# Optimization experiments

Measured on AMD Instinct MI355X. Metric: run time of the kernel, lower is better.

Reference implementation:

```python
import jax, jax.numpy as jnp
import numpy as np


def setup_inputs() -> dict:
    key = jax.random.key(0)
    k1, k2, k3, k4 = jax.random.split(key, 4)
    B, Q, D, H = 8, 512, 4096, 1024
    return {
        "query_embeddings": jax.random.normal(k1, (B, Q, H), dtype=jnp.float32),
        "document_embeddings": jax.random.normal(k2, (B, D, H), dtype=jnp.float32),
        "attention_mask": jax.random.randint(k3, (B, D), 0, 2, dtype=jnp.int32),
        "proj_w": jax.random.normal(k4, (H, H), dtype=jnp.float32) * (H ** -0.5),
        "proj_b": jnp.zeros((H,), dtype=jnp.float32),
    }


def reference(query_embeddings, document_embeddings, attention_mask, proj_w, proj_b):
    H = query_embeddings.shape[-1]
    scale = 1.0 / jnp.sqrt(jnp.asarray(H, dtype=query_embeddings.dtype))
    # Linear projection of queries: [B, Q, H]
    q = jnp.einsum("bqh,hk->bqk", query_embeddings, proj_w) + proj_b
    # Scores: [B, Q, D]
    scores = jnp.einsum("bqh,bdh->bqd", q, document_embeddings) * scale
    # Mask: [B, 1, D]; masked positions -> -inf before softmax
    mask = attention_mask[:, None, :] != 0
    scores = jnp.where(mask, scores, -jnp.inf)
    attention_weights = jax.nn.softmax(scores, axis=-1)
    # Weighted sum over docs: [B, Q, H]
    retrieved_docs = jnp.einsum("bqd,bdh->bqh", attention_weights, document_embeddings)
    return (retrieved_docs, attention_weights)
```

## Files before the change

kernel.cpp:

```cpp
#include <hip/hip_runtime.h>

#define BATCH 8
#define QLEN 512
#define DLEN 4096
#define HDIM 1024

typedef __attribute__((ext_vector_type(8))) short bf16x8;
typedef __attribute__((ext_vector_type(4))) float f32x4;
typedef __attribute__((ext_vector_type(4))) short s16x4;

__device__ __forceinline__ short f2bf(float f) {
    union { float f; unsigned u; } x; x.f = f;
    unsigned r = x.u + 0x7fffu + ((x.u >> 16) & 1u);
    return (short)(r >> 16);
}

__device__ __forceinline__ void gload_lds16(const void* g, void* l) {
    __builtin_amdgcn_global_load_lds(
        (const __attribute__((address_space(1))) unsigned int*)g,
        (__attribute__((address_space(3))) unsigned int*)l,
        16, 0, 0);
}

#define WAIT_VMCNT(n) asm volatile("s_waitcnt vmcnt(" #n ")" ::: "memory")

__global__ void cvt_f32_bf16(const float* __restrict__ in, short* __restrict__ out, int n4) {
    int i = blockIdx.x * blockDim.x + threadIdx.x;
    int stride = gridDim.x * blockDim.x;
    for (; i < n4; i += stride) {
        float4 x = ((const float4*)in)[i];
        s16x4 o = { f2bf(x.x), f2bf(x.y), f2bf(x.z), f2bf(x.w) };
        ((s16x4*)out)[i] = o;
    }
}

__global__ void transpose_w(const float* __restrict__ W, short* __restrict__ Wt) {
    __shared__ float t[32][33];
    const int hb = blockIdx.y * 32, kb = blockIdx.x * 32;
    #pragma unroll
    for (int i = 0; i < 4; ++i) {
        int h = threadIdx.y + i * 8;
        t[h][threadIdx.x] = W[(size_t)(hb + h) * HDIM + kb + threadIdx.x];
    }
    __syncthreads();
    #pragma unroll
    for (int i = 0; i < 4; ++i) {
        int k = threadIdx.y + i * 8;
        Wt[(size_t)(kb + k) * HDIM + hb + threadIdx.x] = f2bf(t[threadIdx.x][k]);
    }
}

__global__ void transpose_docs(const short* __restrict__ docsB, short* __restrict__ docsT) {
    __shared__ unsigned t[64][65];
    const int b = blockIdx.z;
    const int h0 = blockIdx.x * 64, d0 = blockIdx.y * 64;
    const int tq = threadIdx.x & 15;
    const int tr = threadIdx.x >> 4;
    #pragma unroll
    for (int i = 0; i < 4; ++i) {
        int d = tr + i * 16;
        s16x4 v = *(const s16x4*)(docsB + ((size_t)b * DLEN + d0 + d) * HDIM + h0 + tq * 4);
        t[d][tq * 4 + 0] = (unsigned short)v[0];
        t[d][tq * 4 + 1] = (unsigned short)v[1];
        t[d][tq * 4 + 2] = (unsigned short)v[2];
        t[d][tq * 4 + 3] = (unsigned short)v[3];
    }
    __syncthreads();
    #pragma unroll
    for (int i = 0; i < 4; ++i) {
        int h = tr + i * 16;
        s16x4 o = { (short)t[tq * 4 + 0][h], (short)t[tq * 4 + 1][h],
                    (short)t[tq * 4 + 2][h], (short)t[tq * 4 + 3][h] };
        *(s16x4*)(docsT + ((size_t)b * HDIM + h0 + h) * DLEN + d0 + tq * 4) = o;
    }
}

#define G1BM 128
#define G1BN 128
#define G1BK 64

__global__ void gemm128_bias(const short* __restrict__ A, const short* __restrict__ B,
                             short* __restrict__ C, const float* __restrict__ bias,
                             int N, int Kstride, int Kloop, int sx, int sxy) {
    __shared__ short As[G1BM * G1BK];
    __shared__ short Bs[G1BN * G1BK];
    const int tid  = threadIdx.x;
    const int lane = tid & 63;
    const int wv   = tid >> 6;
    const int wr   = wv >> 1, wc = wv & 1;

    const int wg = (blockIdx.x & 7) * (gridDim.x >> 3) + (blockIdx.x >> 3);
    const int bx = wg & ((1 << sx) - 1);
    const int by = (wg >> sx) & ((1 << (sxy - sx)) - 1);

    const size_t rowBase = (size_t)by * G1BM;
    const size_t colBase = (size_t)bx * G1BN;

    f32x4 acc[4][4];
    #pragma unroll
    for (int m = 0; m < 4; ++m)
        #pragma unroll
        for (int n = 0; n < 4; ++n)
            acc[m][n] = (f32x4){0.f, 0.f, 0.f, 0.f};

    const short* aSrc[4]; const short* bSrc[4]; int dOff[4];
    #pragma unroll
    for (int i = 0; i < 4; ++i) {
        const int c = tid + 256 * i;
        const int r = c >> 3, cc = c & 7;
        const int gk = (cc ^ (r & 7)) << 3;
        aSrc[i] = A + (rowBase + r) * (size_t)Kstride + gk;
        bSrc[i] = B + (colBase + r) * (size_t)Kstride + gk;
        dOff[i] = c * 8;
    }
    const int lr = lane & 15;
    const int lk = (lane >> 4) << 3;

    for (int kt = 0; kt < Kloop; kt += G1BK) {
        #pragma unroll
        for (int i = 0; i < 4; ++i) gload_lds16(aSrc[i] + kt, As + dOff[i]);
        #pragma unroll
        for (int i = 0; i < 4; ++i) gload_lds16(bSrc[i] + kt, Bs + dOff[i]);
        __syncthreads();

        #pragma unroll
        for (int kk = 0; kk < 2; ++kk) {
            const int chunkL = (kk * 32 + lk) >> 3;
            bf16x8 af[4], bfr[4];
            #pragma unroll
            for (int m = 0; m < 4; ++m) {
                const int row = wr * 64 + m * 16 + lr;
                af[m] = *(const bf16x8*)(As + row * G1BK + ((chunkL ^ (row & 7)) << 3));
            }
            #pragma unroll
            for (int n = 0; n < 4; ++n) {
                const int row = wc * 64 + n * 16 + lr;
                bfr[n] = *(const bf16x8*)(Bs + row * G1BK + ((chunkL ^ (row & 7)) << 3));
            }
            #pragma unroll
            for (int m = 0; m < 4; ++m)
                #pragma unroll
                for (int n = 0; n < 4; ++n)
                    acc[m][n] = __builtin_amdgcn_mfma_f32_16x16x32_bf16(af[m], bfr[n], acc[m][n], 0, 0, 0);
        }
        __syncthreads();
    }

    const int orow = (lane >> 4) << 2;
    const int ocol = lane & 15;
    #pragma unroll
    for (int n = 0; n < 4; ++n) {
        const size_t col = colBase + wc * 64 + n * 16 + ocol;
        const float bv = bias[col];
        #pragma unroll
        for (int m = 0; m < 4; ++m) {
            const size_t rbase = rowBase + wr * 64 + m * 16 + orow;
            #pragma unroll
            for (int j = 0; j < 4; ++j)
                C[(rbase + j) * (size_t)N + col] = f2bf(acc[m][n][j] + bv);
        }
    }
}

#define G2BM 256
#define G2BN 256
#define G2BK 32
#define G2TS (G2BM * G2BK)

template<int EPI>
__launch_bounds__(512, 1)
__global__ void gemm256(const short* __restrict__ A, const short* __restrict__ B,
                        float* __restrict__ Cv, float scale,
                        int N, int Kstride, int Kloop, int kOffStep,
                        int sx, int sxy,
                        long long aB, long long bB, long long cB) {
    __shared__ short As[3 * G2TS];
    __shared__ short Bs[3 * G2TS];
    const int tid  = threadIdx.x;
    const int lane = tid & 63;
    const int wv   = tid >> 6;
    const int wm   = wv >> 2;
    const int wn   = wv & 3;

    const int wg = (blockIdx.x & 7) * (gridDim.x >> 3) + (blockIdx.x >> 3);
    const int bx = wg & ((1 << sx) - 1);
    const int by = (wg >> sx) & ((1 << (sxy - sx)) - 1);
    const int z  = wg >> sxy;

    const size_t rowBase = (size_t)by * G2BM;
    const size_t colBase = (size_t)bx * G2BN;
    const int bb = z & 7;
    const int kOff = (z >> 3) * kOffStep;
    const short* Ag = A + (size_t)bb * aB + kOff;
    const short* Bg = B + (size_t)bb * bB + kOff;

    f32x4 acc[8][4];
    #pragma unroll
    for (int m = 0; m < 8; ++m)
        #pragma unroll
        for (int n = 0; n < 4; ++n)
            acc[m][n] = (f32x4){0.f, 0.f, 0.f, 0.f};

    const short* aSrc[2]; const short* bSrc[2]; int dOff[2];
    #pragma unroll
    for (int i = 0; i < 2; ++i) {
        const int c = tid + 512 * i;
        const int r = c >> 2, cc = c & 3;
        const int gk = (cc ^ ((r >> 1) & 3)) << 3;
        aSrc[i] = Ag + (rowBase + r) * (size_t)Kstride + gk;
        bSrc[i] = Bg + (colBase + r) * (size_t)Kstride + gk;
        dOff[i] = c * 8;
    }
    const int chunkL = lane >> 4;
    const int lr = lane & 15;

    const int nt = Kloop / G2BK;

    #pragma unroll
    for (int i = 0; i < 2; ++i) gload_lds16(aSrc[i], As + dOff[i]);
    #pragma unroll
    for (int i = 0; i < 2; ++i) gload_lds16(bSrc[i], Bs + dOff[i]);
    #pragma unroll
    for (int i = 0; i < 2; ++i) gload_lds16(aSrc[i] + G2BK, As + G2TS + dOff[i]);
    #pragma unroll
    for (int i = 0; i < 2; ++i) gload_lds16(bSrc[i] + G2BK, Bs + G2TS + dOff[i]);
    WAIT_VMCNT(4);
    __builtin_amdgcn_s_barrier();

    for (int t = 0; t < nt; ++t) {
        if (t + 2 < nt) {
            const int kt = (t + 2) * G2BK;
            const int o = ((t + 2) % 3) * G2TS;
            #pragma unroll
            for (int i = 0; i < 2; ++i) gload_lds16(aSrc[i] + kt, As + o + dOff[i]);
            #pragma unroll
            for (int i = 0; i < 2; ++i) gload_lds16(bSrc[i] + kt, Bs + o + dOff[i]);
        }

        const short* Ab = As + (t % 3) * G2TS;
        const short* Bb = Bs + (t % 3) * G2TS;
        bf16x8 bfr[4], af[8];
        #pragma unroll
        for (int n = 0; n < 4; ++n) {
            const int row = wn * 64 + n * 16 + lr;
            bfr[n] = *(const bf16x8*)(Bb + row * G2BK + ((chunkL ^ ((row >> 1) & 3)) << 3));
        }
        #pragma unroll
        for (int m = 0; m < 8; ++m) {
            const int row = wm * 128 + m * 16 + lr;
            af[m] = *(const bf16x8*)(Ab + row * G2BK + ((chunkL ^ ((row >> 1) & 3)) << 3));
        }
        #pragma unroll
        for (int m = 0; m < 8; ++m)
            #pragma unroll
            for (int n = 0; n < 4; ++n)
                acc[m][n] = __builtin_amdgcn_mfma_f32_16x16x32_bf16(af[m], bfr[n], acc[m][n], 0, 0, 0);

        if (t + 1 < nt) {
            if (t + 2 < nt) { WAIT_VMCNT(4); }
            else           { WAIT_VMCNT(0); }
            __builtin_amdgcn_sched_barrier(0);
            __builtin_amdgcn_s_barrier();
            __builtin_amdgcn_sched_barrier(0);
        }
    }

    const int orow = (lane >> 4) << 2;
    const int ocol = lane & 15;
    #pragma unroll
    for (int n = 0; n < 4; ++n) {
        const size_t col = colBase + wn * 64 + n * 16 + ocol;
        #pragma unroll
        for (int m = 0; m < 8; ++m) {
            const size_t rbase = rowBase + wm * 128 + m * 16 + orow;
            #pragma unroll
            for (int j = 0; j < 4; ++j) {
                const float v = acc[m][n][j];
                const size_t off = (size_t)z * cB + (rbase + j) * (size_t)N + col;
                Cv[off] = (EPI == 1) ? v * scale : v;
            }
        }
    }
}

__global__ void reduce4(const float* __restrict__ p, float* __restrict__ out, int n4) {
    int i = blockIdx.x * blockDim.x + threadIdx.x;
    const int stride = gridDim.x * blockDim.x;
    const float4* p4 = (const float4*)p;
    float4* o4 = (float4*)out;
    for (; i < n4; i += stride) {
        float4 a = p4[i];
        float4 b = p4[i + 1048576];
        float4 c = p4[i + 2097152];
        float4 d = p4[i + 3145728];
        float4 r;
        r.x = a.x + b.x + c.x + d.x;
        r.y = a.y + b.y + c.y + d.y;
        r.z = a.z + b.z + c.z + d.z;
        r.w = a.w + b.w + c.w + d.w;
        o4[i] = r;
    }
}

__global__ void softmax_rows(const float* __restrict__ scores, const int* __restrict__ mask,
                             float* __restrict__ attnF, short* __restrict__ attnB) {
    const int row = blockIdx.x;
    const int b   = row >> 9;
    const int tid = threadIdx.x;
    const int lane = tid & 63;
    const int wv = tid >> 6;
    const float4* S  = (const float4*)(scores + (size_t)row * DLEN);
    const int4*   Mk = (const int4*)(mask + (size_t)b * DLEN);
    __shared__ float red[8];

    float v[16];
    float mx = -INFINITY;
    #pragma unroll
    for (int i = 0; i < 4; ++i) {
        float4 s = S[i * 256 + tid];
        int4   m = Mk[i * 256 + tid];
        v[i * 4 + 0] = m.x ? s.x : -INFINITY;
        v[i * 4 + 1] = m.y ? s.y : -INFINITY;
        v[i * 4 + 2] = m.z ? s.z : -INFINITY;
        v[i * 4 + 3] = m.w ? s.w : -INFINITY;
        #pragma unroll
        for (int c = 0; c < 4; ++c) mx = fmaxf(mx, v[i * 4 + c]);
    }
    #pragma unroll
    for (int o = 32; o > 0; o >>= 1) mx = fmaxf(mx, __shfl_xor(mx, o));
    if (lane == 0) red[wv] = mx;
    __syncthreads();
    mx = fmaxf(fmaxf(red[0], red[1]), fmaxf(red[2], red[3]));

    float sum = 0.f;
    #pragma unroll
    for (int i = 0; i < 16; ++i) {
        float e = __expf(v[i] - mx);
        v[i] = e;
        sum += e;
    }
    #pragma unroll
    for (int o = 32; o > 0; o >>= 1) sum += __shfl_xor(sum, o);
    __syncthreads();
    if (lane == 0) red[4 + wv] = sum;
    __syncthreads();
    sum = red[4] + red[5] + red[6] + red[7];
    const float inv = 1.0f / sum;

    float4* OF = (float4*)(attnF + (size_t)row * DLEN);
    s16x4*  OB = (s16x4*)(attnB + (size_t)row * DLEN);
    #pragma unroll
    for (int i = 0; i < 4; ++i) {
        float4 w;
        w.x = v[i * 4 + 0] * inv;
        w.y = v[i * 4 + 1] * inv;
        w.z = v[i * 4 + 2] * inv;
        w.w = v[i * 4 + 3] * inv;
        OF[i * 256 + tid] = w;
        s16x4 o = { f2bf(w.x), f2bf(w.y), f2bf(w.z), f2bf(w.w) };
        OB[i * 256 + tid] = o;
    }
}

extern "C" void kernel_launch(void* const* d_in, const int* in_sizes, int n_in,
                              void* d_out, int out_size, void* d_ws, size_t ws_size,
                              hipStream_t stream) {
    const float* qe   = (const float*)d_in[0];
    const float* docs = (const float*)d_in[1];
    const int*   mask = (const int*)d_in[2];
    const float* pw   = (const float*)d_in[3];
    const float* pb   = (const float*)d_in[4];

    float* outRet  = (float*)d_out;
    float* outAttn = outRet + (size_t)BATCH * QLEN * HDIM;

    char* ws = (char*)d_ws;
    short* qeB   = (short*)(ws + 0);
    short* wt    = (short*)(ws + 8388608);
    short* qpB   = (short*)(ws + 10485760);
    short* docsB = (short*)(ws + 18874368);
    short* docsT = (short*)(ws + 85983232);
    float* scor  = (float*)(ws + 153092096);
    short* attnB = (short*)(ws + 220200960);

    cvt_f32_bf16<<<dim3(1024), dim3(256), 0, stream>>>(qe, qeB, (BATCH * QLEN * HDIM) / 4);
    cvt_f32_bf16<<<dim3(2048), dim3(256), 0, stream>>>(docs, docsB, (BATCH * DLEN * HDIM) / 4);
    transpose_w<<<dim3(32, 32), dim3(32, 8), 0, stream>>>(pw, wt);
    transpose_docs<<<dim3(HDIM / 64, DLEN / 64, BATCH), dim3(256), 0, stream>>>(docsB, docsT);

    gemm128_bias<<<dim3(256), dim3(256), 0, stream>>>(
        qeB, wt, qpB, pb, HDIM, HDIM, HDIM, 3, 8);

    gemm256<1><<<dim3(256), dim3(512), 0, stream>>>(
        qpB, docsB, scor, 0.03125f, DLEN, HDIM, HDIM, 0, 4, 5,
        (long long)QLEN * HDIM, (long long)DLEN * HDIM, (long long)QLEN * DLEN);

    softmax_rows<<<dim3(BATCH * QLEN), dim3(256), 0, stream>>>(scor, mask, outAttn, attnB);

    gemm256<2><<<dim3(256), dim3(512), 0, stream>>>(
        attnB, docsT, scor, 1.f, HDIM, DLEN, DLEN / 4, DLEN / 4, 2, 3,
        (long long)QLEN * DLEN, (long long)HDIM * DLEN, (long long)QLEN * HDIM);

    reduce4<<<dim3(2048), dim3(256), 0, stream>>>(scor, outRet, (BATCH * QLEN * HDIM) / 4);
}
```

Measured before the change: 427.6 us.

## Deepen GEMM LDS pipelines to four stages and pipeline the projection GEMM

```diff
diff --git a/kernel.cpp b/kernel.cpp
--- a/kernel.cpp
+++ b/kernel.cpp
@@ -76,14 +76,14 @@
 }
 
 #define G1BM 128
-#define G1BN 128
-#define G1BK 64
+#define G1BK 32
+#define G1TS (G1BM * G1BK)
 
 __global__ void gemm128_bias(const short* __restrict__ A, const short* __restrict__ B,
                              short* __restrict__ C, const float* __restrict__ bias,
                              int N, int Kstride, int Kloop, int sx, int sxy) {
-    __shared__ short As[G1BM * G1BK];
-    __shared__ short Bs[G1BN * G1BK];
+    __shared__ short As[4 * G1TS];
+    __shared__ short Bs[4 * G1TS];
     const int tid  = threadIdx.x;
     const int lane = tid & 63;
     const int wv   = tid >> 6;
@@ -94,7 +94,7 @@
     const int by = (wg >> sx) & ((1 << (sxy - sx)) - 1);
 
     const size_t rowBase = (size_t)by * G1BM;
-    const size_t colBase = (size_t)bx * G1BN;
+    const size_t colBase = (size_t)bx * G1BM;
 
     f32x4 acc[4][4];
     #pragma unroll
@@ -103,47 +103,68 @@
         for (int n = 0; n < 4; ++n)
             acc[m][n] = (f32x4){0.f, 0.f, 0.f, 0.f};
 
-    const short* aSrc[4]; const short* bSrc[4]; int dOff[4];
-    #pragma unroll
-    for (int i = 0; i < 4; ++i) {
+    const short* aSrc[2]; const short* bSrc[2]; int dOff[2];
+    #pragma unroll
+    for (int i = 0; i < 2; ++i) {
         const int c = tid + 256 * i;
-        const int r = c >> 3, cc = c & 7;
-        const int gk = (cc ^ (r & 7)) << 3;
+        const int r = c >> 2, cc = c & 3;
+        const int gk = (cc ^ ((r >> 1) & 3)) << 3;
         aSrc[i] = A + (rowBase + r) * (size_t)Kstride + gk;
         bSrc[i] = B + (colBase + r) * (size_t)Kstride + gk;
         dOff[i] = c * 8;
     }
+    const int chunkL = lane >> 4;
     const int lr = lane & 15;
-    const int lk = (lane >> 4) << 3;
-
-    for (int kt = 0; kt < Kloop; kt += G1BK) {
-        #pragma unroll
-        for (int i = 0; i < 4; ++i) gload_lds16(aSrc[i] + kt, As + dOff[i]);
-        #pragma unroll
-        for (int i = 0; i < 4; ++i) gload_lds16(bSrc[i] + kt, Bs + dOff[i]);
-        __syncthreads();
-
-        #pragma unroll
-        for (int kk = 0; kk < 2; ++kk) {
-            const int chunkL = (kk * 32 + lk) >> 3;
-            bf16x8 af[4], bfr[4];
-            #pragma unroll
-            for (int m = 0; m < 4; ++m) {
-                const int row = wr * 64 + m * 16 + lr;
-                af[m] = *(const bf16x8*)(As + row * G1BK + ((chunkL ^ (row & 7)) << 3));
-            }
-            #pragma unroll
-            for (int n = 0; n < 4; ++n) {
-                const int row = wc * 64 + n * 16 + lr;
-                bfr[n] = *(const bf16x8*)(Bs + row * G1BK + ((chunkL ^ (row & 7)) << 3));
-            }
-            #pragma unroll
-            for (int m = 0; m < 4; ++m)
-                #pragma unroll
-                for (int n = 0; n < 4; ++n)
-                    acc[m][n] = __builtin_amdgcn_mfma_f32_16x16x32_bf16(af[m], bfr[n], acc[m][n], 0, 0, 0);
-        }
-        __syncthreads();
+
+    const int nt = Kloop / G1BK;
+
+    #pragma unroll
+    for (int s = 0; s < 3; ++s) {
+        #pragma unroll
+        for (int i = 0; i < 2; ++i) gload_lds16(aSrc[i] + s * G1BK, As + s * G1TS + dOff[i]);
+        #pragma unroll
+        for (int i = 0; i < 2; ++i) gload_lds16(bSrc[i] + s * G1BK, Bs + s * G1TS + dOff[i]);
+    }
+    WAIT_VMCNT(8);
+    __builtin_amdgcn_s_barrier();
+
+    for (int t = 0; t < nt; ++t) {
+        if (t + 3 < nt) {
+            const int kt = (t + 3) * G1BK;
+            const int o = ((t + 3) & 3) * G1TS;
+            #pragma unroll
+            for (int i = 0; i < 2; ++i) gload_lds16(aSrc[i] + kt, As + o + dOff[i]);
+            #pragma unroll
+            for (int i = 0; i < 2; ++i) gload_lds16(bSrc[i] + kt, Bs + o + dOff[i]);
+        }
+
+        const short* Ab = As + (t & 3) * G1TS;
+        const short* Bb = Bs + (t & 3) * G1TS;
+        bf16x8 af[4], bfr[4];
+        #pragma unroll
+        for (int m = 0; m < 4; ++m) {
+            const int row = wr * 64 + m * 16 + lr;
+            af[m] = *(const bf16x8*)(Ab + row * G1BK + ((chunkL ^ ((row >> 1) & 3)) << 3));
+        }
+        #pragma unroll
+        for (int n = 0; n < 4; ++n) {
+            const int row = wc * 64 + n * 16 + lr;
+            bfr[n] = *(const bf16x8*)(Bb + row * G1BK + ((chunkL ^ ((row >> 1) & 3)) << 3));
+        }
+        #pragma unroll
+        for (int m = 0; m < 4; ++m)
+            #pragma unroll
+            for (int n = 0; n < 4; ++n)
+                acc[m][n] = __builtin_amdgcn_mfma_f32_16x16x32_bf16(af[m], bfr[n], acc[m][n], 0, 0, 0);
+
+        if (t + 1 < nt) {
+            if (t + 3 < nt)      { WAIT_VMCNT(8); }
+            else if (t + 2 < nt) { WAIT_VMCNT(4); }
+            else                 { WAIT_VMCNT(0); }
+            __builtin_amdgcn_sched_barrier(0);
+            __builtin_amdgcn_s_barrier();
+            __builtin_amdgcn_sched_barrier(0);
+        }
     }
 
     const int orow = (lane >> 4) << 2;
@@ -163,7 +184,6 @@
 }
 
 #define G2BM 256
-#define G2BN 256
 #define G2BK 32
 #define G2TS (G2BM * G2BK)
 
@@ -174,8 +194,8 @@
                         int N, int Kstride, int Kloop, int kOffStep,
                         int sx, int sxy,
                         long long aB, long long bB, long long cB) {
-    __shared__ short As[3 * G2TS];
-    __shared__ short Bs[3 * G2TS];
+    __shared__ short As[4 * G2TS];
+    __shared__ short Bs[4 * G2TS];
     const int tid  = threadIdx.x;
     const int lane = tid & 63;
     const int wv   = tid >> 6;
@@ -188,7 +208,7 @@
     const int z  = wg >> sxy;
 
     const size_t rowBase = (size_t)by * G2BM;
-    const size_t colBase = (size_t)bx * G2BN;
+    const size_t colBase = (size_t)bx * G2BM;
     const int bb = z & 7;
     const int kOff = (z >> 3) * kOffStep;
     const short* Ag = A + (size_t)bb * aB + kOff;
@@ -217,28 +237,27 @@
     const int nt = Kloop / G2BK;
 
     #pragma unroll
-    for (int i = 0; i < 2; ++i) gload_lds16(aSrc[i], As + dOff[i]);
-    #pragma unroll
-    for (int i = 0; i < 2; ++i) gload_lds16(bSrc[i], Bs + dOff[i]);
-    #pragma unroll
-    for (int i = 0; i < 2; ++i) gload_lds16(aSrc[i] + G2BK, As + G2TS + dOff[i]);
-    #pragma unroll
-    for (int i = 0; i < 2; ++i) gload_lds16(bSrc[i] + G2BK, Bs + G2TS + dOff[i]);
-    WAIT_VMCNT(4);
+    for (int s = 0; s < 3; ++s) {
+        #pragma unroll
+        for (int i = 0; i < 2; ++i) gload_lds16(aSrc[i] + s * G2BK, As + s * G2TS + dOff[i]);
+        #pragma unroll
+        for (int i = 0; i < 2; ++i) gload_lds16(bSrc[i] + s * G2BK, Bs + s * G2TS + dOff[i]);
+    }
+    WAIT_VMCNT(8);
     __builtin_amdgcn_s_barrier();
 
     for (int t = 0; t < nt; ++t) {
-        if (t + 2 < nt) {
-            const int kt = (t + 2) * G2BK;
-            const int o = ((t + 2) % 3) * G2TS;
+        if (t + 3 < nt) {
+            const int kt = (t + 3) * G2BK;
+            const int o = ((t + 3) & 3) * G2TS;
             #pragma unroll
             for (int i = 0; i < 2; ++i) gload_lds16(aSrc[i] + kt, As + o + dOff[i]);
             #pragma unroll
             for (int i = 0; i < 2; ++i) gload_lds16(bSrc[i] + kt, Bs + o + dOff[i]);
         }
 
-        const short* Ab = As + (t % 3) * G2TS;
-        const short* Bb = Bs + (t % 3) * G2TS;
+        const short* Ab = As + (t & 3) * G2TS;
+        const short* Bb = Bs + (t & 3) * G2TS;
         bf16x8 bfr[4], af[8];
         #pragma unroll
         for (int n = 0; n < 4; ++n) {
@@ -257,8 +276,9 @@
                 acc[m][n] = __builtin_amdgcn_mfma_f32_16x16x32_bf16(af[m], bfr[n], acc[m][n], 0, 0, 0);
 
         if (t + 1 < nt) {
-            if (t + 2 < nt) { WAIT_VMCNT(4); }
-            else           { WAIT_VMCNT(0); }
+            if (t + 3 < nt)      { WAIT_VMCNT(8); }
+            else if (t + 2 < nt) { WAIT_VMCNT(4); }
+            else                 { WAIT_VMCNT(0); }
             __builtin_amdgcn_sched_barrier(0);
             __builtin_amdgcn_s_barrier();
             __builtin_amdgcn_sched_barrier(0);
```

Result: no change. 431.2 us (+0.8%).
